# Kernel optimization log

Measured on AMD Instinct MI355X. Metric: run time of the kernel, lower is better.

The kernel has to match this reference:

```python
import jax, jax.numpy as jnp
import numpy as np
import math

D_MODEL = 1024
N_HEAD = 16


def setup_inputs() -> dict:
    key = jax.random.key(0)
    ks = jax.random.split(key, 11)
    B, S, D = 2, 2048, D_MODEL
    s = 1.0 / math.sqrt(D)
    return {
        "q": jax.random.normal(ks[0], (B, S, D), dtype=jnp.float32),
        "k": jax.random.normal(ks[1], (B, S, D), dtype=jnp.float32),
        "v": jax.random.normal(ks[2], (B, S, D), dtype=jnp.float32),
        "w_q": jax.random.normal(ks[3], (D, D), dtype=jnp.float32) * s,
        "b_q": jnp.zeros((D,), dtype=jnp.float32),
        "w_k": jax.random.normal(ks[4], (D, D), dtype=jnp.float32) * s,
        "b_k": jnp.zeros((D,), dtype=jnp.float32),
        "w_v": jax.random.normal(ks[5], (D, D), dtype=jnp.float32) * s,
        "b_v": jnp.zeros((D,), dtype=jnp.float32),
        "w_out": jax.random.normal(ks[6], (D, D), dtype=jnp.float32) * s,
        "b_out": jnp.zeros((D,), dtype=jnp.float32),
    }


def _split_heads(x, n_head):
    B, S, D = x.shape
    return x.reshape(B, S, n_head, D // n_head).transpose(0, 2, 1, 3)  # [B,H,S,dk]


def reference(q, k, v, w_q, b_q, w_k, b_k, w_v, b_v, w_out, b_out):
    # Linear projections (weights stored as [in, out])
    qh = _split_heads(q @ w_q + b_q, N_HEAD)
    kh = _split_heads(k @ w_k + b_k, N_HEAD)
    vh = _split_heads(v @ w_v + b_v, N_HEAD)
    d_k = qh.shape[-1]
    scores = jnp.einsum("bhqd,bhkd->bhqk", qh, kh) / jnp.sqrt(jnp.float32(d_k))
    attn = jax.nn.softmax(scores, axis=-1)
    context = jnp.einsum("bhqk,bhkd->bhqd", attn, vh)  # [B,H,S,dk]
    B, H, S, dk = context.shape
    context = context.transpose(0, 2, 1, 3).reshape(B, S, H * dk)
    return context @ w_out + b_out
```

## Files before the change

kernel.cpp:

```cpp
#include <hip/hip_runtime.h>
#include <hip/hip_bf16.h>


typedef __bf16 bf16x8 __attribute__((ext_vector_type(8)));
typedef float  f32x4  __attribute__((ext_vector_type(4)));

#define DEVI __device__ __forceinline__
#define SWZ(row, cb) ((cb) ^ (((row) & 7) << 4))

#define GLOAD16(gsrc, ldst)                                                    \
    __builtin_amdgcn_global_load_lds(                                          \
        (const __attribute__((address_space(1))) unsigned int*)(gsrc),         \
        (__attribute__((address_space(3))) unsigned int*)(ldst), 16, 0, 0)

#define BAR()        asm volatile("s_barrier" ::: "memory")
#define WAIT_LGKM0() asm volatile("s_waitcnt lgkmcnt(0)" ::: "memory")
#define WAIT_VM0()   asm volatile("s_waitcnt vmcnt(0)" ::: "memory")
#define WAIT_VM2()   asm volatile("s_waitcnt vmcnt(2)" ::: "memory")

static DEVI unsigned short f2bf(float f) {
    __hip_bfloat16 h = __float2bfloat16(f);
    return __builtin_bit_cast(unsigned short, h);
}
static DEVI unsigned int pack2(float a, float b) {
    return (unsigned int)f2bf(a) | ((unsigned int)f2bf(b) << 16);
}
static DEVI unsigned int cvt2(float lo, float hi) {
    unsigned int r;
    asm("v_cvt_pk_bf16_f32 %0, %1, %2" : "=v"(r) : "v"(lo), "v"(hi));
    return r;
}
static DEVI float bf2f(unsigned int lo16) {
    unsigned int x = lo16 << 16;
    return __builtin_bit_cast(float, x);
}
static DEVI bf16x8 ldsRead(const char* p) {
    return __builtin_bit_cast(bf16x8, *(const uint4*)p);
}

__global__ __launch_bounds__(256) void wtrans_kernel(
    const float* w0, const float* w1, const float* w2, const float* w3,
    unsigned short* t0, unsigned short* t1, unsigned short* t2, unsigned short* t3)
{
    __shared__ unsigned short tile[64][80];
    const int z = blockIdx.z;
    const float* w = (z == 0) ? w0 : (z == 1) ? w1 : (z == 2) ? w2 : w3;
    unsigned short* wt = (z == 0) ? t0 : (z == 1) ? t1 : (z == 2) ? t2 : t3;
    const int n0 = blockIdx.x * 64, k0 = blockIdx.y * 64;
    const int t = threadIdx.x;
#pragma unroll
    for (int i = 0; i < 4; i++) {
        int chunk = t + i * 256;
        int row = chunk >> 4, c4 = chunk & 15;
        float4 v = *(const float4*)(w + (size_t)(k0 + row) * 1024 + n0 + c4 * 4);
        tile[c4 * 4 + 0][row] = f2bf(v.x);
        tile[c4 * 4 + 1][row] = f2bf(v.y);
        tile[c4 * 4 + 2][row] = f2bf(v.z);
        tile[c4 * 4 + 3][row] = f2bf(v.w);
    }
    __syncthreads();
#pragma unroll
    for (int i = 0; i < 2; i++) {
        int idx = t + i * 256;
        int row = idx >> 3, ch = idx & 7;
        uint4 vv = *(const uint4*)(&tile[row][ch * 8]);
        *(uint4*)(wt + (size_t)(n0 + row) * 1024 + k0 + ch * 8) = vv;
    }
}

__global__ __launch_bounds__(256, 3) void gemm_proj_kernel(
    const float* x0, const float* x1, const float* x2,
    const unsigned short* wt0, const unsigned short* wt1, const unsigned short* wt2,
    const float* b0, const float* b1, const float* b2,
    unsigned short* y0, unsigned short* y1, unsigned short* y2)
{
    __shared__ __align__(16) char Af[32768];
    __shared__ __align__(16) char Bs[16384];
    const int i = blockIdx.x;
    const int xcd = i & 7, j = i >> 3;
    const int panel = xcd * 12 + (j >> 3);
    const int z = panel >> 5, mblk = panel & 31;
    const int n0 = (j & 7) * 128, m0 = mblk * 128;

    const float* X = (z == 0) ? x0 : (z == 1) ? x1 : x2;
    const unsigned short* Wt = (z == 0) ? wt0 : (z == 1) ? wt1 : wt2;
    const float* bias = (z == 0) ? b0 : (z == 1) ? b1 : b2;
    unsigned short* Y = (z == 0) ? y0 : (z == 1) ? y1 : y2;
    const float scale = (z == 0) ? 0.125f * 1.44269504f : 1.0f;
    const int t = threadIdx.x, w = t >> 6, l = t & 63, l15 = l & 15, l4 = l >> 4;
    const int wr = w >> 1, wc = w & 1;
    const char* Ab = (const char*)X;
    const char* Bb = (const char*)Wt;

    f32x4 acc[4][4];
#pragma unroll
    for (int mr = 0; mr < 4; mr++)
#pragma unroll
        for (int nc = 0; nc < 4; nc++) acc[mr][nc] = f32x4{0.f, 0.f, 0.f, 0.f};

#pragma unroll 1
    for (int k = 0; k < 16; ++k) {
        const int k0 = k * 64;
        BAR();
#pragma unroll
        for (int jj = 0; jj < 8; jj++) {
            int o = w * 8192 + jj * 1024 + l * 16;
            int row = o >> 8, cb = (o >> 4) & 15;
            int csw = cb ^ ((row & 7) << 1);
            GLOAD16(Ab + ((size_t)(m0 + row) * 1024 + k0 + csw * 4) * 4,
                    Af + w * 8192 + jj * 1024);
        }
#pragma unroll
        for (int jj = 0; jj < 4; jj++) {
            int o = w * 4096 + jj * 1024 + l * 16;
            int row = o >> 7, cb = (o >> 4) & 7;
            int csw = cb ^ (row & 7);
            GLOAD16(Bb + ((size_t)(n0 + row) * 1024 + k0 + csw * 8) * 2,
                    Bs + w * 4096 + jj * 1024);
        }
        WAIT_VM0();
        BAR();

        bf16x8 af[4][2], bfr[4][2];
#pragma unroll
        for (int mr = 0; mr < 4; mr++) {
            int row = wr * 64 + mr * 16 + l15;
            int x = (row & 7) << 1;
#pragma unroll
            for (int kf = 0; kf < 2; kf++) {
                int cb = kf * 8 + l4 * 2;
                const char* p = Af + row * 256 + (cb ^ x) * 16;
                float4 a = *(const float4*)p;
                float4 b = *(const float4*)(p + 16);
                uint4 pk = {cvt2(a.x, a.y), cvt2(a.z, a.w),
                            cvt2(b.x, b.y), cvt2(b.z, b.w)};
                af[mr][kf] = __builtin_bit_cast(bf16x8, pk);
            }
        }
#pragma unroll
        for (int nc = 0; nc < 4; nc++) {
            int row = wc * 64 + nc * 16 + l15;
#pragma unroll
            for (int kf = 0; kf < 2; kf++)
                bfr[nc][kf] = ldsRead(Bs + row * 128 + SWZ(row, kf * 64 + l4 * 16));
        }
        __builtin_amdgcn_s_setprio(1);
#pragma unroll
        for (int kf = 0; kf < 2; kf++)
#pragma unroll
            for (int mr = 0; mr < 4; mr++)
#pragma unroll
                for (int nc = 0; nc < 4; nc++)
                    acc[mr][nc] = __builtin_amdgcn_mfma_f32_16x16x32_bf16(
                        af[mr][kf], bfr[nc][kf], acc[mr][nc], 0, 0, 0);
        __builtin_amdgcn_s_setprio(0);
    }

    WAIT_LGKM0();
    BAR();
    char* Es = Af;
    if (z < 2) {
#pragma unroll
        for (int nc = 0; nc < 4; nc++) {
            float bv = bias[n0 + wc * 64 + nc * 16 + l15];
#pragma unroll
            for (int mr = 0; mr < 4; mr++) {
#pragma unroll
                for (int r = 0; r < 2; r++) {
                    int mloc = wr * 64 + mr * 16 + l4 * 4 + r * 2;
                    int nloc = wc * 64 + nc * 16 + l15;
                    unsigned int pk = cvt2((acc[mr][nc][r * 2] + bv) * scale,
                                           (acc[mr][nc][r * 2 + 1] + bv) * scale);
                    *(unsigned short*)(Es + mloc * 256 + nloc * 2) =
                        (unsigned short)(pk & 0xffff);
                    *(unsigned short*)(Es + (mloc + 1) * 256 + nloc * 2) =
                        (unsigned short)(pk >> 16);
                }
            }
        }
        WAIT_LGKM0();
        BAR();
#pragma unroll
        for (int ii = 0; ii < 8; ii++) {
            int idx = t + ii * 256, row = idx >> 4, ch = idx & 15;
            *(uint4*)((char*)Y + ((size_t)(m0 + row) * 1024 + n0 + ch * 8) * 2) =
                *(const uint4*)(Es + row * 256 + ch * 16);
        }
    } else {
#pragma unroll
        for (int nc = 0; nc < 4; nc++) {
            float bv = bias[n0 + wc * 64 + nc * 16 + l15];
#pragma unroll
            for (int mr = 0; mr < 4; mr++) {
#pragma unroll
                for (int r = 0; r < 2; r++) {
                    int mloc = wr * 64 + mr * 16 + l4 * 4 + r * 2;
                    int nloc = wc * 64 + nc * 16 + l15;
                    unsigned int pk = cvt2(acc[mr][nc][r * 2] + bv,
                                           acc[mr][nc][r * 2 + 1] + bv);
                    *(unsigned int*)(Es + nloc * 256 + mloc * 2) = pk;
                }
            }
        }
        WAIT_LGKM0();
        BAR();
        const int bb = m0 >> 11, s0 = m0 & 2047;
#pragma unroll
        for (int ii = 0; ii < 8; ii++) {
            int idx = t + ii * 256, row = idx >> 4, ch = idx & 15;
            int col = n0 + row, h = col >> 6, d = col & 63;
            *(uint4*)((char*)Y +
                      (((size_t)((bb * 16 + h) * 64 + d)) * 2048 + s0 + ch * 8) * 2) =
                *(const uint4*)(Es + row * 256 + ch * 16);
        }
    }
}

__global__ __launch_bounds__(256, 4) void attn_kernel(
    const unsigned short* Q2, const unsigned short* K2, const unsigned short* VT,
    unsigned short* Opart, float* lpart)
{
    __shared__ __align__(16) char sm[40960];
    char* Pall = sm;
    char* K0s = sm + 16384;
    char* K1s = sm + 24576;
    char* Vs  = sm + 32768;
    const int t = threadIdx.x, w = t >> 6, l = t & 63, l15 = l & 15, l4 = l >> 4;
    char* Ps = Pall + w * 4096;

    const int i = blockIdx.x;
    const int xcd = i & 7, j = i >> 3;
    const int bh = xcd * 4 + (j >> 5);
    const int jj = j & 31, qblk = jj >> 1, kh = jj & 1;
    const int b = bh >> 4, h = bh & 15;
    const int q0 = qblk * 128;
    const char* Qb = (const char*)(Q2 + ((size_t)(b * 2048 + q0)) * 1024 + h * 64);
    const char* Kb = (const char*)(K2 + ((size_t)(b * 2048)) * 1024 + h * 64);
    const char* Vb = (const char*)(VT + (size_t)bh * 64 * 2048);

    int kGO[2], vGO[2];
#pragma unroll
    for (int jj2 = 0; jj2 < 2; jj2++) {
        int row = w * 16 + jj2 * 8 + (l >> 3);
        int ch = (l & 7) ^ (row & 7);
        kGO[jj2] = row * 2048 + ch * 16;
        vGO[jj2] = row * 4096 + ch * 16;
    }
    int kRO[4][2];
#pragma unroll
    for (int cc = 0; cc < 4; cc++) {
        int row = cc * 16 + l15;
#pragma unroll
        for (int kf = 0; kf < 2; kf++)
            kRO[cc][kf] = row * 128 + SWZ(row, kf * 64 + l4 * 16);
    }
    int pWO[2][4], pRO[2][2];
#pragma unroll
    for (int qi = 0; qi < 2; qi++) {
        int row = qi * 16 + l15;
#pragma unroll
        for (int cc = 0; cc < 4; cc++) {
            int c = (cc * 2 + (l4 >> 1)) ^ (l15 & 7);
            pWO[qi][cc] = row * 128 + c * 16 + (l4 & 1) * 8;
        }
#pragma unroll
        for (int kf = 0; kf < 2; kf++)
            pRO[qi][kf] = row * 128 + SWZ(row, kf * 64 + l4 * 16);
    }

#define STAGE_K(TT, Kdst)                                                      \
    do {                                                                       \
        int kk0 = (TT) * 64;                                                   \
        _Pragma("unroll") for (int s2 = 0; s2 < 2; s2++)                       \
            GLOAD16(Kb + (size_t)(kk0 * 2048 + kGO[s2]),                       \
                    (Kdst) + w * 2048 + s2 * 1024);                            \
    } while (0)
#define STAGE_V(TT)                                                            \
    do {                                                                       \
        int kk0 = (TT) * 64;                                                   \
        _Pragma("unroll") for (int s2 = 0; s2 < 2; s2++)                       \
            GLOAD16(Vb + (size_t)(kk0 * 2 + vGO[s2]),                          \
                    Vs + w * 2048 + s2 * 1024);                                \
    } while (0)

    bf16x8 qf[2][2];
#pragma unroll
    for (int qi = 0; qi < 2; qi++) {
        int row = w * 32 + qi * 16 + l15;
#pragma unroll
        for (int kf = 0; kf < 2; kf++)
            qf[qi][kf] = __builtin_bit_cast(
                bf16x8, *(const uint4*)(Qb + (size_t)row * 2048 + kf * 64 + l4 * 16));
    }

    const int tbase = kh * 16;
    STAGE_K(tbase + (qblk & 15), K0s);
    STAGE_V(tbase + (qblk & 15));
    WAIT_VM0();
    BAR();

    bf16x8 ones;
#pragma unroll
    for (int e = 0; e < 8; e++) ones[e] = (__bf16)1.0f;

    f32x4 o[2][4], ol[2];
#pragma unroll
    for (int qi = 0; qi < 2; qi++) {
#pragma unroll
        for (int c = 0; c < 4; c++) o[qi][c] = f32x4{0.f, 0.f, 0.f, 0.f};
        ol[qi] = f32x4{0.f, 0.f, 0.f, 0.f};
    }

#pragma unroll 1
    for (int it = 0; it < 16; it++) {
        char* Kc = (it & 1) ? K1s : K0s;
        char* Kn = (it & 1) ? K0s : K1s;
        if (it < 15) STAGE_K(tbase + ((qblk + it + 1) & 15), Kn);

        f32x4 sacc[2][4];
#pragma unroll
        for (int qi = 0; qi < 2; qi++)
#pragma unroll
            for (int c = 0; c < 4; c++) sacc[qi][c] = f32x4{0.f, 0.f, 0.f, 0.f};
        __builtin_amdgcn_s_setprio(1);
#pragma unroll
        for (int cc = 0; cc < 4; cc++)
#pragma unroll
            for (int kf = 0; kf < 2; kf++) {
                bf16x8 kfrag = ldsRead(Kc + kRO[cc][kf]);
#pragma unroll
                for (int qi = 0; qi < 2; qi++)
                    sacc[qi][cc] = __builtin_amdgcn_mfma_f32_16x16x32_bf16(
                        kfrag, qf[qi][kf], sacc[qi][cc], 0, 0, 0);
            }
        __builtin_amdgcn_s_setprio(0);

#pragma unroll
        for (int qi = 0; qi < 2; qi++)
#pragma unroll
            for (int cc = 0; cc < 4; cc++)
#pragma unroll
                for (int r = 0; r < 4; r++)
                    sacc[qi][cc][r] = __builtin_amdgcn_exp2f(sacc[qi][cc][r]);

#pragma unroll
        for (int qi = 0; qi < 2; qi++)
#pragma unroll
            for (int cc = 0; cc < 4; cc++) {
                uint2 pk = {cvt2(sacc[qi][cc][0], sacc[qi][cc][1]),
                            cvt2(sacc[qi][cc][2], sacc[qi][cc][3])};
                *(uint2*)(Ps + pWO[qi][cc]) = pk;
            }
        asm volatile("" ::: "memory");
        bf16x8 pf[2][2];
#pragma unroll
        for (int qi = 0; qi < 2; qi++)
#pragma unroll
            for (int kf = 0; kf < 2; kf++)
                pf[qi][kf] = ldsRead(Ps + pRO[qi][kf]);

        if (it < 15) { WAIT_VM2(); } else { WAIT_VM0(); }
        BAR();

        __builtin_amdgcn_s_setprio(1);
#pragma unroll
        for (int dd = 0; dd < 4; dd++)
#pragma unroll
            for (int kf = 0; kf < 2; kf++) {
                bf16x8 vfrag = ldsRead(Vs + kRO[dd][kf]);
#pragma unroll
                for (int qi = 0; qi < 2; qi++)
                    o[qi][dd] = __builtin_amdgcn_mfma_f32_16x16x32_bf16(
                        vfrag, pf[qi][kf], o[qi][dd], 0, 0, 0);
            }
#pragma unroll
        for (int qi = 0; qi < 2; qi++)
#pragma unroll
            for (int kf = 0; kf < 2; kf++)
                ol[qi] = __builtin_amdgcn_mfma_f32_16x16x32_bf16(
                    ones, pf[qi][kf], ol[qi], 0, 0, 0);
        __builtin_amdgcn_s_setprio(0);

        WAIT_LGKM0();
        BAR();
        if (it < 15) {
            STAGE_V(tbase + ((qblk + it + 1) & 15));
            WAIT_VM2();
            BAR();
        }
    }
#undef STAGE_K
#undef STAGE_V

    const size_t qgbase = (size_t)bh * 2048 + q0 + w * 32;
#pragma unroll
    for (int qi = 0; qi < 2; qi++) {
        size_t qg = qgbase + qi * 16 + l15;
        unsigned short* orow = Opart + ((size_t)kh * 65536 + qg) * 64;
#pragma unroll
        for (int dd = 0; dd < 4; dd++) {
            uint2 pk = {cvt2(o[qi][dd][0], o[qi][dd][1]),
                        cvt2(o[qi][dd][2], o[qi][dd][3])};
            *(uint2*)(orow + dd * 16 + l4 * 4) = pk;
        }
        if (l4 == 0) lpart[(size_t)kh * 65536 + qg] = ol[qi][0];
    }
}

__global__ __launch_bounds__(256) void reduce_kernel(
    const unsigned short* Op, const float* lp, unsigned short* ctx)
{
    int idx = blockIdx.x * 256 + threadIdx.x;
    int qg = idx >> 3, c8 = idx & 7;
    uint4 a = *(const uint4*)(Op + (size_t)qg * 64 + c8 * 8);
    uint4 bq = *(const uint4*)(Op + (size_t)65536 * 64 + (size_t)qg * 64 + c8 * 8);
    float rinv = 1.0f / (lp[qg] + lp[65536 + qg]);
    const unsigned int* pa = (const unsigned int*)&a;
    const unsigned int* pb = (const unsigned int*)&bq;
    unsigned int outp[4];
#pragma unroll
    for (int j = 0; j < 4; j++) {
        float s0 = (bf2f(pa[j] & 0xffff) + bf2f(pb[j] & 0xffff)) * rinv;
        float s1 = (bf2f(pa[j] >> 16) + bf2f(pb[j] >> 16)) * rinv;
        outp[j] = cvt2(s0, s1);
    }
    int bh = qg >> 11, s = qg & 2047, b = bh >> 4, h = bh & 15;
    *(uint4*)(ctx + ((size_t)(b * 2048 + s)) * 1024 + h * 64 + c8 * 8) =
        *(const uint4*)outp;
}

__global__ __launch_bounds__(256, 3) void gemm_out_kernel(
    const unsigned short* ctx, const unsigned short* wto, const float* bias, float* out)
{
    __shared__ __align__(16) char As[16384];
    __shared__ __align__(16) char Bs[16384];
    const int i = blockIdx.x;
    const int xcd = i & 7, j = i >> 3;
    const int mpanel = xcd * 4 + (j >> 3);
    const int n0 = (j & 7) * 128, m0 = mpanel * 128;
    const int t = threadIdx.x, w = t >> 6, l = t & 63, l15 = l & 15, l4 = l >> 4;
    const int wr = w >> 1, wc = w & 1;
    const char* Ab = (const char*)ctx;
    const char* Bb = (const char*)wto;

    f32x4 acc[4][4];
#pragma unroll
    for (int mr = 0; mr < 4; mr++)
#pragma unroll
        for (int nc = 0; nc < 4; nc++) acc[mr][nc] = f32x4{0.f, 0.f, 0.f, 0.f};

#pragma unroll 1
    for (int k = 0; k < 16; ++k) {
        const int k0 = k * 64;
        BAR();
#pragma unroll
        for (int jj = 0; jj < 4; jj++) {
            int o = w * 4096 + jj * 1024 + l * 16;
            int row = o >> 7, cb = (o >> 4) & 7;
            int csw = cb ^ (row & 7);
            GLOAD16(Ab + ((size_t)(m0 + row) * 1024 + k0 + csw * 8) * 2,
                    As + w * 4096 + jj * 1024);
        }
#pragma unroll
        for (int jj = 0; jj < 4; jj++) {
            int o = w * 4096 + jj * 1024 + l * 16;
            int row = o >> 7, cb = (o >> 4) & 7;
            int csw = cb ^ (row & 7);
            GLOAD16(Bb + ((size_t)(n0 + row) * 1024 + k0 + csw * 8) * 2,
                    Bs + w * 4096 + jj * 1024);
        }
        WAIT_VM0();
        BAR();

        bf16x8 af[4][2], bfr[4][2];
#pragma unroll
        for (int mr = 0; mr < 4; mr++) {
            int row = wr * 64 + mr * 16 + l15;
#pragma unroll
            for (int kf = 0; kf < 2; kf++)
                af[mr][kf] = ldsRead(As + row * 128 + SWZ(row, kf * 64 + l4 * 16));
        }
#pragma unroll
        for (int nc = 0; nc < 4; nc++) {
            int row = wc * 64 + nc * 16 + l15;
#pragma unroll
            for (int kf = 0; kf < 2; kf++)
                bfr[nc][kf] = ldsRead(Bs + row * 128 + SWZ(row, kf * 64 + l4 * 16));
        }
        __builtin_amdgcn_s_setprio(1);
#pragma unroll
        for (int kf = 0; kf < 2; kf++)
#pragma unroll
            for (int mr = 0; mr < 4; mr++)
#pragma unroll
                for (int nc = 0; nc < 4; nc++)
                    acc[mr][nc] = __builtin_amdgcn_mfma_f32_16x16x32_bf16(
                        af[mr][kf], bfr[nc][kf], acc[mr][nc], 0, 0, 0);
        __builtin_amdgcn_s_setprio(0);
    }

#pragma unroll
    for (int nc = 0; nc < 4; nc++) {
        int col = n0 + wc * 64 + nc * 16 + l15;
        float bv = bias[col];
#pragma unroll
        for (int mr = 0; mr < 4; mr++)
#pragma unroll
            for (int r = 0; r < 4; r++) {
                int m = m0 + wr * 64 + mr * 16 + l4 * 4 + r;
                out[(size_t)m * 1024 + col] = acc[mr][nc][r] + bv;
            }
    }
}

extern "C" void kernel_launch(void* const* d_in, const int* in_sizes, int n_in,
                              void* d_out, int out_size, void* d_ws, size_t ws_size,
                              hipStream_t stream)
{
    (void)in_sizes; (void)n_in; (void)out_size; (void)ws_size;
    const float* q  = (const float*)d_in[0];
    const float* k  = (const float*)d_in[1];
    const float* v  = (const float*)d_in[2];
    const float* wq = (const float*)d_in[3];
    const float* bq = (const float*)d_in[4];
    const float* wk = (const float*)d_in[5];
    const float* bk = (const float*)d_in[6];
    const float* wv = (const float*)d_in[7];
    const float* bv = (const float*)d_in[8];
    const float* wo = (const float*)d_in[9];
    const float* bo = (const float*)d_in[10];

    char* ws = (char*)d_ws;
    const size_t MB = 1u << 20;
    unsigned short* WTq = (unsigned short*)(ws + 0 * MB);
    unsigned short* WTk = (unsigned short*)(ws + 2 * MB);
    unsigned short* WTv = (unsigned short*)(ws + 4 * MB);
    unsigned short* WTo = (unsigned short*)(ws + 6 * MB);
    unsigned short* Q2  = (unsigned short*)(ws + 8 * MB);
    unsigned short* K2  = (unsigned short*)(ws + 16 * MB);
    unsigned short* VT  = (unsigned short*)(ws + 24 * MB);
    unsigned short* CTX = (unsigned short*)(ws + 32 * MB);
    unsigned short* OPART = (unsigned short*)(ws + 40 * MB);
    float*          LPART = (float*)(ws + 57 * MB);

    wtrans_kernel<<<dim3(16, 16, 4), 256, 0, stream>>>(wq, wk, wv, wo, WTq, WTk, WTv, WTo);
    gemm_proj_kernel<<<768, 256, 0, stream>>>(q, k, v, WTq, WTk, WTv,
                                              bq, bk, bv, Q2, K2, VT);
    attn_kernel<<<1024, 256, 0, stream>>>(Q2, K2, VT, OPART, LPART);
    reduce_kernel<<<2048, 256, 0, stream>>>(OPART, LPART, CTX);
    gemm_out_kernel<<<256, 256, 0, stream>>>(CTX, WTo, bo, (float*)d_out);
}
```

Baseline: 117.9 us.

## Pre-convert activations to bf16 in separate kernel before projection GEMM

Adds a standalone kernel that converts the fp32 q/k/v activations to bf16 into workspace buffers. The projection GEMM then loads bf16 tiles, which halves A-tile LDS usage and drops the in-loop fp32-to-bf16 conversion, and occupancy is raised to 4 blocks per SM. The cost is an extra kernel launch plus a full fp32 read and bf16 write/read of the activations. The new buffers reuse workspace that the attention partials later overwrite.

```diff
diff --git a/kernel.cpp b/kernel.cpp
--- a/kernel.cpp
+++ b/kernel.cpp
@@ -22,9 +22,6 @@
     __hip_bfloat16 h = __float2bfloat16(f);
     return __builtin_bit_cast(unsigned short, h);
 }
-static DEVI unsigned int pack2(float a, float b) {
-    return (unsigned int)f2bf(a) | ((unsigned int)f2bf(b) << 16);
-}
 static DEVI unsigned int cvt2(float lo, float hi) {
     unsigned int r;
     asm("v_cvt_pk_bf16_f32 %0, %1, %2" : "=v"(r) : "v"(lo), "v"(hi));
@@ -36,6 +33,20 @@
 }
 static DEVI bf16x8 ldsRead(const char* p) {
     return __builtin_bit_cast(bf16x8, *(const uint4*)p);
+}
+
+__global__ __launch_bounds__(256) void xconv_kernel(
+    const float* x0, const float* x1, const float* x2,
+    unsigned short* y0, unsigned short* y1, unsigned short* y2)
+{
+    const int z = blockIdx.y;
+    const float* x = (z == 0) ? x0 : (z == 1) ? x1 : x2;
+    unsigned short* y = (z == 0) ? y0 : (z == 1) ? y1 : y2;
+    size_t idx = ((size_t)blockIdx.x * 256 + threadIdx.x) * 8;
+    float4 a = *(const float4*)(x + idx);
+    float4 b = *(const float4*)(x + idx + 4);
+    uint4 pk = {cvt2(a.x, a.y), cvt2(a.z, a.w), cvt2(b.x, b.y), cvt2(b.z, b.w)};
+    *(uint4*)(y + idx) = pk;
 }
 
 __global__ __launch_bounds__(256) void wtrans_kernel(
@@ -68,21 +79,22 @@
     }
 }
 
-__global__ __launch_bounds__(256, 3) void gemm_proj_kernel(
-    const float* x0, const float* x1, const float* x2,
+__global__ __launch_bounds__(256, 4) void gemm_proj_kernel(
+    const unsigned short* x0, const unsigned short* x1, const unsigned short* x2,
     const unsigned short* wt0, const unsigned short* wt1, const unsigned short* wt2,
     const float* b0, const float* b1, const float* b2,
     unsigned short* y0, unsigned short* y1, unsigned short* y2)
 {
-    __shared__ __align__(16) char Af[32768];
-    __shared__ __align__(16) char Bs[16384];
+    __shared__ __align__(16) char sm[32768];
+    char* As = sm;
+    char* Bs = sm + 16384;
     const int i = blockIdx.x;
     const int xcd = i & 7, j = i >> 3;
     const int panel = xcd * 12 + (j >> 3);
     const int z = panel >> 5, mblk = panel & 31;
     const int n0 = (j & 7) * 128, m0 = mblk * 128;
 
-    const float* X = (z == 0) ? x0 : (z == 1) ? x1 : x2;
+    const unsigned short* X = (z == 0) ? x0 : (z == 1) ? x1 : x2;
     const unsigned short* Wt = (z == 0) ? wt0 : (z == 1) ? wt1 : wt2;
     const float* bias = (z == 0) ? b0 : (z == 1) ? b1 : b2;
     unsigned short* Y = (z == 0) ? y0 : (z == 1) ? y1 : y2;
@@ -103,12 +115,12 @@
         const int k0 = k * 64;
         BAR();
 #pragma unroll
-        for (int jj = 0; jj < 8; jj++) {
-            int o = w * 8192 + jj * 1024 + l * 16;
-            int row = o >> 8, cb = (o >> 4) & 15;
-            int csw = cb ^ ((row & 7) << 1);
-            GLOAD16(Ab + ((size_t)(m0 + row) * 1024 + k0 + csw * 4) * 4,
-                    Af + w * 8192 + jj * 1024);
+        for (int jj = 0; jj < 4; jj++) {
+            int o = w * 4096 + jj * 1024 + l * 16;
+            int row = o >> 7, cb = (o >> 4) & 7;
+            int csw = cb ^ (row & 7);
+            GLOAD16(Ab + ((size_t)(m0 + row) * 1024 + k0 + csw * 8) * 2,
+                    As + w * 4096 + jj * 1024);
         }
 #pragma unroll
         for (int jj = 0; jj < 4; jj++) {
@@ -125,17 +137,9 @@
 #pragma unroll
         for (int mr = 0; mr < 4; mr++) {
             int row = wr * 64 + mr * 16 + l15;
-            int x = (row & 7) << 1;
-#pragma unroll
-            for (int kf = 0; kf < 2; kf++) {
-                int cb = kf * 8 + l4 * 2;
-                const char* p = Af + row * 256 + (cb ^ x) * 16;
-                float4 a = *(const float4*)p;
-                float4 b = *(const float4*)(p + 16);
-                uint4 pk = {cvt2(a.x, a.y), cvt2(a.z, a.w),
-                            cvt2(b.x, b.y), cvt2(b.z, b.w)};
-                af[mr][kf] = __builtin_bit_cast(bf16x8, pk);
-            }
+#pragma unroll
+            for (int kf = 0; kf < 2; kf++)
+                af[mr][kf] = ldsRead(As + row * 128 + SWZ(row, kf * 64 + l4 * 16));
         }
 #pragma unroll
         for (int nc = 0; nc < 4; nc++) {
@@ -158,7 +162,7 @@
 
     WAIT_LGKM0();
     BAR();
-    char* Es = Af;
+    char* Es = sm;
     if (z < 2) {
 #pragma unroll
         for (int nc = 0; nc < 4; nc++) {
@@ -540,11 +544,15 @@
     unsigned short* K2  = (unsigned short*)(ws + 16 * MB);
     unsigned short* VT  = (unsigned short*)(ws + 24 * MB);
     unsigned short* CTX = (unsigned short*)(ws + 32 * MB);
+    unsigned short* X2q = (unsigned short*)(ws + 40 * MB);
+    unsigned short* X2k = (unsigned short*)(ws + 48 * MB);
+    unsigned short* X2v = (unsigned short*)(ws + 56 * MB);
     unsigned short* OPART = (unsigned short*)(ws + 40 * MB);
-    float*          LPART = (float*)(ws + 57 * MB);
+    float*          LPART = (float*)(ws + 56 * MB);
 
     wtrans_kernel<<<dim3(16, 16, 4), 256, 0, stream>>>(wq, wk, wv, wo, WTq, WTk, WTv, WTo);
-    gemm_proj_kernel<<<768, 256, 0, stream>>>(q, k, v, WTq, WTk, WTv,
+    xconv_kernel<<<dim3(2048, 3), 256, 0, stream>>>(q, k, v, X2q, X2k, X2v);
+    gemm_proj_kernel<<<768, 256, 0, stream>>>(X2q, X2k, X2v, WTq, WTk, WTv,
                                               bq, bk, bv, Q2, K2, VT);
     attn_kernel<<<1024, 256, 0, stream>>>(Q2, K2, VT, OPART, LPART);
     reduce_kernel<<<2048, 256, 0, stream>>>(OPART, LPART, CTX);
```

Measured after the change: 159.0 us. 34.8% more time.

## Fuse split-KV partial reduction into output projection GEMM A-tile loading

Applied to the files above, without the earlier changes.

Removes the separate reduce kernel and instead has the output GEMM read both attention partial outputs and their row sums, combine and normalize them in registers, and write the bf16 result into the swizzled A tile in shared memory. This drops one launch and the write-then-read round trip of the intermediate context buffer. In exchange, each A tile reduction is recomputed by every N-tile block, A traffic doubles (two partials plus sums), and the A loads become synchronous register loads instead of async global-to-LDS copies.

```diff
diff --git a/kernel.cpp b/kernel.cpp
--- a/kernel.cpp
+++ b/kernel.cpp
@@ -21,9 +21,6 @@
 static DEVI unsigned short f2bf(float f) {
     __hip_bfloat16 h = __float2bfloat16(f);
     return __builtin_bit_cast(unsigned short, h);
-}
-static DEVI unsigned int pack2(float a, float b) {
-    return (unsigned int)f2bf(a) | ((unsigned int)f2bf(b) << 16);
 }
 static DEVI unsigned int cvt2(float lo, float hi) {
     unsigned int r;
@@ -407,30 +404,9 @@
     }
 }
 
-__global__ __launch_bounds__(256) void reduce_kernel(
-    const unsigned short* Op, const float* lp, unsigned short* ctx)
-{
-    int idx = blockIdx.x * 256 + threadIdx.x;
-    int qg = idx >> 3, c8 = idx & 7;
-    uint4 a = *(const uint4*)(Op + (size_t)qg * 64 + c8 * 8);
-    uint4 bq = *(const uint4*)(Op + (size_t)65536 * 64 + (size_t)qg * 64 + c8 * 8);
-    float rinv = 1.0f / (lp[qg] + lp[65536 + qg]);
-    const unsigned int* pa = (const unsigned int*)&a;
-    const unsigned int* pb = (const unsigned int*)&bq;
-    unsigned int outp[4];
-#pragma unroll
-    for (int j = 0; j < 4; j++) {
-        float s0 = (bf2f(pa[j] & 0xffff) + bf2f(pb[j] & 0xffff)) * rinv;
-        float s1 = (bf2f(pa[j] >> 16) + bf2f(pb[j] >> 16)) * rinv;
-        outp[j] = cvt2(s0, s1);
-    }
-    int bh = qg >> 11, s = qg & 2047, b = bh >> 4, h = bh & 15;
-    *(uint4*)(ctx + ((size_t)(b * 2048 + s)) * 1024 + h * 64 + c8 * 8) =
-        *(const uint4*)outp;
-}
-
 __global__ __launch_bounds__(256, 3) void gemm_out_kernel(
-    const unsigned short* ctx, const unsigned short* wto, const float* bias, float* out)
+    const unsigned short* Op, const float* lp, const unsigned short* wto,
+    const float* bias, float* out)
 {
     __shared__ __align__(16) char As[16384];
     __shared__ __align__(16) char Bs[16384];
@@ -440,8 +416,19 @@
     const int n0 = (j & 7) * 128, m0 = mpanel * 128;
     const int t = threadIdx.x, w = t >> 6, l = t & 63, l15 = l & 15, l4 = l >> 4;
     const int wr = w >> 1, wc = w & 1;
-    const char* Ab = (const char*)ctx;
     const char* Bb = (const char*)wto;
+
+    size_t qb[4];
+    int rowv[4], chv[4];
+#pragma unroll
+    for (int ii = 0; ii < 4; ii++) {
+        int idx = t + ii * 256;
+        rowv[ii] = idx >> 3;
+        chv[ii] = idx & 7;
+        int m = m0 + rowv[ii];
+        int bb = m >> 11, s = m & 2047;
+        qb[ii] = (size_t)bb * 32768 + s;
+    }
 
     f32x4 acc[4][4];
 #pragma unroll
@@ -453,14 +440,6 @@
     for (int k = 0; k < 16; ++k) {
         const int k0 = k * 64;
         BAR();
-#pragma unroll
-        for (int jj = 0; jj < 4; jj++) {
-            int o = w * 4096 + jj * 1024 + l * 16;
-            int row = o >> 7, cb = (o >> 4) & 7;
-            int csw = cb ^ (row & 7);
-            GLOAD16(Ab + ((size_t)(m0 + row) * 1024 + k0 + csw * 8) * 2,
-                    As + w * 4096 + jj * 1024);
-        }
 #pragma unroll
         for (int jj = 0; jj < 4; jj++) {
             int o = w * 4096 + jj * 1024 + l * 16;
@@ -469,7 +448,27 @@
             GLOAD16(Bb + ((size_t)(n0 + row) * 1024 + k0 + csw * 8) * 2,
                     Bs + w * 4096 + jj * 1024);
         }
+#pragma unroll
+        for (int ii = 0; ii < 4; ii++) {
+            size_t qg = qb[ii] + (size_t)k * 2048;
+            const unsigned short* p0 = Op + qg * 64 + chv[ii] * 8;
+            uint4 a0 = *(const uint4*)p0;
+            uint4 a1 = *(const uint4*)(p0 + (size_t)65536 * 64);
+            float rinv = 1.0f / (lp[qg] + lp[65536 + qg]);
+            const unsigned int* pa = (const unsigned int*)&a0;
+            const unsigned int* pb = (const unsigned int*)&a1;
+            unsigned int pk[4];
+#pragma unroll
+            for (int jq = 0; jq < 4; jq++) {
+                float s0 = (bf2f(pa[jq] & 0xffff) + bf2f(pb[jq] & 0xffff)) * rinv;
+                float s1 = (bf2f(pa[jq] >> 16) + bf2f(pb[jq] >> 16)) * rinv;
+                pk[jq] = cvt2(s0, s1);
+            }
+            *(uint4*)(As + rowv[ii] * 128 + SWZ(rowv[ii], chv[ii] * 16)) =
+                *(const uint4*)pk;
+        }
         WAIT_VM0();
+        WAIT_LGKM0();
         BAR();
 
         bf16x8 af[4][2], bfr[4][2];
@@ -497,6 +496,7 @@
                     acc[mr][nc] = __builtin_amdgcn_mfma_f32_16x16x32_bf16(
                         af[mr][kf], bfr[nc][kf], acc[mr][nc], 0, 0, 0);
         __builtin_amdgcn_s_setprio(0);
+        WAIT_LGKM0();
     }
 
 #pragma unroll
@@ -539,7 +539,6 @@
     unsigned short* Q2  = (unsigned short*)(ws + 8 * MB);
     unsigned short* K2  = (unsigned short*)(ws + 16 * MB);
     unsigned short* VT  = (unsigned short*)(ws + 24 * MB);
-    unsigned short* CTX = (unsigned short*)(ws + 32 * MB);
     unsigned short* OPART = (unsigned short*)(ws + 40 * MB);
     float*          LPART = (float*)(ws + 57 * MB);
 
@@ -547,6 +546,5 @@
     gemm_proj_kernel<<<768, 256, 0, stream>>>(q, k, v, WTq, WTk, WTv,
                                               bq, bk, bv, Q2, K2, VT);
     attn_kernel<<<1024, 256, 0, stream>>>(Q2, K2, VT, OPART, LPART);
-    reduce_kernel<<<2048, 256, 0, stream>>>(OPART, LPART, CTX);
-    gemm_out_kernel<<<256, 256, 0, stream>>>(CTX, WTo, bo, (float*)d_out);
-}
+    gemm_out_kernel<<<256, 256, 0, stream>>>(OPART, LPART, WTo, bo, (float*)d_out);
+}
```

After: 128.1 us. 1.09x slower.
